# Kernel tuning notes

Measured on AMD Instinct MI355X. Metric: run time of the kernel, lower is better.

The kernel has to match this reference:

```python
import jax, jax.numpy as jnp
import numpy as np

B, S, D_MODEL, D_MEM, N_HEADS, NU = 8, 2048, 1024, 1024, 16, 3
D_HEAD = D_MODEL // N_HEADS            # 64
D_KEY = 2 * NU * (D_MEM // N_HEADS)    # 384


def _to_heads(x, n_heads):
    b, s, d = x.shape
    return x.reshape(b, s, n_heads, d // n_heads).transpose(0, 2, 1, 3)


def _dpfp(x, nu):
    # Deterministic Positive Feature Projection: (..., d) -> (..., 2*nu*d)
    x = jnp.concatenate([jax.nn.relu(x), jax.nn.relu(-x)], axis=-1)
    rolled = jnp.concatenate([jnp.roll(x, j, axis=-1) for j in range(1, nu + 1)], axis=-1)
    rep = jnp.concatenate([x] * nu, axis=-1)
    return rep * rolled


def setup_inputs() -> dict:
    key = jax.random.key(0)
    k0, k1, k2, k3, k4 = jax.random.split(key, 5)
    mem_tokens = jax.random.normal(k0, (B, S, D_MODEL), dtype=jnp.float32)
    # nn.Linear(in, out) weight shape is [out, in]
    W_mk = jax.random.normal(k1, (D_MEM, D_MODEL), dtype=jnp.float32) * 0.02
    W_mv = jax.random.normal(k2, (D_MODEL, D_MODEL), dtype=jnp.float32) * 0.02
    W_mb = jax.random.normal(k3, (D_MODEL, D_MODEL), dtype=jnp.float32) * 0.02
    W_mem = jax.random.normal(k4, (B, N_HEADS, D_KEY, D_HEAD), dtype=jnp.float32) * 0.01
    z = jnp.ones((B, N_HEADS, D_KEY), dtype=jnp.float32)
    return {"mem_tokens": mem_tokens, "W_mk": W_mk, "W_mv": W_mv, "W_mb": W_mb,
            "W_mem": W_mem, "z": z}


def reference(mem_tokens, W_mk, W_mv, W_mb, W_mem, z):
    # key projection + DPFP feature map
    k = _to_heads(mem_tokens @ W_mk.T, N_HEADS)          # [b,h,s,d_mem/h]
    mk = _dpfp(k, NU)                                     # [b,h,s,d_key]
    norm = jnp.linalg.norm(mk, axis=-1, keepdims=True)
    mk = mk / jnp.maximum(norm, 1e-12)                    # F.normalize(p=2)

    new_mv = _to_heads(mem_tokens @ W_mv.T, N_HEADS)      # [b,h,s,d_head]

    # retrieve previous values (first_seg=False, use_denom=True path)
    num = jnp.einsum('bhsk,bhkd->bhsd', mk, W_mem)
    denom = jnp.einsum('bhk,bhsk->bhs', z, mk)[..., None] + 1e-5
    prev_mv = num / denom

    mv = new_mv - prev_mv
    mb = _to_heads(jax.nn.sigmoid(mem_tokens @ W_mb.T), N_HEADS)

    # gating=True einsum: 'ihjk,ihjt,ihjt->ihkt'
    associations = jnp.einsum('bhsk,bhsd,bhsd->bhkd', mk, mv, mb)
    return W_mem + associations
```

## Files before the change

kernel.cpp:

```cpp
#include <hip/hip_runtime.h>
#include <hip/hip_bf16.h>

#define B_ 8
#define S_ 2048
#define DM 1024
#define H_ 16
#define DH 64
#define DK 384

#define AS3 __attribute__((address_space(3)))
#define AS1 __attribute__((address_space(1)))
typedef unsigned int u32;

typedef __attribute__((ext_vector_type(8))) short bf16x8;
typedef __attribute__((ext_vector_type(4))) short bf16x4;
typedef __attribute__((ext_vector_type(4))) float f32x4;

static __device__ __forceinline__ ushort f2b(float f) {
  __hip_bfloat16 h = __float2bfloat16(f);
  return *reinterpret_cast<ushort*>(&h);
}
static __device__ __forceinline__ float b2f(ushort u) {
  __hip_bfloat16 h;
  *reinterpret_cast<ushort*>(&h) = u;
  return __bfloat162float(h);
}

__global__ __launch_bounds__(256) void k_cvt(
    const float* __restrict__ X, const float* __restrict__ Wk,
    const float* __restrict__ Wv, const float* __restrict__ Wb,
    ushort* __restrict__ Xb, ushort* __restrict__ Wball) {
  const int total = 2097152 + 3 * 131072;
  int c = blockIdx.x * 256 + threadIdx.x;
  const int stride = gridDim.x * 256;
  for (; c < total; c += stride) {
    const float* s;
    ushort* d;
    size_t off;
    if (c < 2097152) { s = X; d = Xb; off = (size_t)c; }
    else {
      int cc = c - 2097152;
      int wsel = cc >> 17;
      off = (size_t)(cc & 131071);
      s = wsel == 0 ? Wk : (wsel == 1 ? Wv : Wb);
      d = Wball + (size_t)wsel * (DM * DM);
    }
    float4 a = *(const float4*)(s + off * 8);
    float4 b = *(const float4*)(s + off * 8 + 4);
    ushort u[8] = { f2b(a.x), f2b(a.y), f2b(a.z), f2b(a.w),
                    f2b(b.x), f2b(b.y), f2b(b.z), f2b(b.w) };
    *(uint4*)(d + off * 8) = *(uint4*)u;
  }
}

__global__ __launch_bounds__(256) void k_proj(
    const ushort* __restrict__ Xb, const ushort* __restrict__ Wball,
    ushort* __restrict__ kvb) {
  __shared__ ushort SH[4 * 8192];
  const int t = threadIdx.x, lane = t & 63, w = t >> 6;
  const int wm = w >> 1, wn = w & 1;
  const int l15 = lane & 15, lq = lane >> 4;
  const int bid = blockIdx.x + (blockIdx.y << 7) + (blockIdx.z << 10);
  const int c = bid & 7, r = bid >> 3;
  const int zb = r >> 7;
  const int rem = r & 127;
  const int mgrp = rem >> 3;
  const int nb = rem & 7;
  const int m0 = (c * 16 + mgrp) * 128;
  const int n0 = nb * 128;
  const int wsel = zb;
  const ushort* Wmat = Wball + (size_t)wsel * (DM * DM);
  ushort* out = kvb + (size_t)wsel * ((size_t)B_ * H_ * S_ * DH);

  const int rowst = (lane >> 3);
  const int colsw = ((lane & 7) ^ rowst) << 3;

  const ushort* pX[4];
  const ushort* pW[4];
  #pragma unroll
  for (int j = 0; j < 4; j++) {
    int row = (w * 4 + j) * 8 + rowst;
    pX[j] = Xb + (size_t)(m0 + row) * DM + colsw;
    pW[j] = Wmat + (size_t)(n0 + row) * DM + colsw;
  }
  ushort* dA = SH + w * 2048;
  ushort* dB = SH + 16384 + w * 2048;

  auto STAGE = [&](int buf, int kidx) {
    #pragma unroll
    for (int j = 0; j < 4; j++) {
      __builtin_amdgcn_global_load_lds(
          (const AS1 u32*)(pX[j] + kidx * 64),
          (AS3 u32*)(dA + buf * 8192 + j * 512), 16, 0, 0);
      __builtin_amdgcn_global_load_lds(
          (const AS1 u32*)(pW[j] + kidx * 64),
          (AS3 u32*)(dB + buf * 8192 + j * 512), 16, 0, 0);
    }
  };

  const int aoffb = (wm * 64 + l15) * 64;
  const int boffb = (wn * 64 + l15) * 64;
  const int csw0 = (lq ^ (lane & 7)) << 3;
  const int csw1 = ((lq + 4) ^ (lane & 7)) << 3;

  f32x4 acc[4][4] = {};
  STAGE(0, 0);
  __syncthreads();
  #pragma unroll
  for (int kt = 0; kt < 16; kt++) {
    const int cur = kt & 1;
    if (kt < 15) STAGE(cur ^ 1, kt + 1);
    const int ab = cur * 8192;
    #pragma unroll
    for (int kk2 = 0; kk2 < 2; kk2++) {
      const int csw = kk2 ? csw1 : csw0;
      bf16x8 af[4], bfr[4];
      #pragma unroll
      for (int mi = 0; mi < 4; mi++)
        af[mi] = *(const bf16x8*)&SH[ab + aoffb + mi * 1024 + csw];
      #pragma unroll
      for (int ni = 0; ni < 4; ni++)
        bfr[ni] = *(const bf16x8*)&SH[16384 + ab + boffb + ni * 1024 + csw];
      #pragma unroll
      for (int mi = 0; mi < 4; mi++)
        #pragma unroll
        for (int ni = 0; ni < 4; ni++)
          acc[mi][ni] = __builtin_amdgcn_mfma_f32_16x16x32_bf16(af[mi], bfr[ni], acc[mi][ni], 0, 0, 0);
    }
    __syncthreads();
  }

  ushort (*Cb)[136] = (ushort (*)[136])SH;
  #pragma unroll
  for (int mi = 0; mi < 4; mi++)
    #pragma unroll
    for (int ni = 0; ni < 4; ni++)
      #pragma unroll
      for (int rr = 0; rr < 4; rr++) {
        float val = acc[mi][ni][rr];
        if (wsel == 2) val = 1.0f / (1.0f + __expf(-val));
        Cb[wm * 64 + mi * 16 + lq * 4 + rr][wn * 64 + ni * 16 + l15] = f2b(val);
      }
  __syncthreads();
  #pragma unroll
  for (int q = 0; q < 8; q++) {
    int idx = q * 256 + t;
    int lm = idx >> 4;
    int c16 = idx & 15;
    int m = m0 + lm;
    int b = m >> 11, s = m & 2047;
    int o0 = n0 + c16 * 8;
    int h = o0 >> 6, d = o0 & 63;
    *(uint4*)(out + (((size_t)(b * H_ + h)) * S_ + s) * DH + d) =
        *(uint4*)&Cb[lm][c16 * 8];
  }
}

__global__ __launch_bounds__(512) void k_fused6(
    const ushort* __restrict__ Kb, const ushort* __restrict__ Vb,
    const ushort* __restrict__ Bgb, const float* __restrict__ Wmem,
    const float* __restrict__ z, ushort* __restrict__ part) {
  __shared__ u32 mkLd[32][192];
  __shared__ ushort mkT[384][36];
  __shared__ ushort gLT[64][36];
  __shared__ ushort zL[384];
  const int t = threadIdx.x, l = t & 63, w = t >> 6;
  const int l15 = l & 15, lq = l >> 4;
  const int bh = blockIdx.y, seg = blockIdx.x;
  const size_t rowbase = (size_t)bh * S_;
  const int mi = w >> 2, ni = w & 3;
  const int dcol = ni * 16 + l15;

  for (int cc = t; cc < DK; cc += 512) {
    int u = cc >> 7, p = (cc & 127) >> 1, par = cc & 1;
    zL[cc] = f2b(z[(size_t)bh * DK + u * 128 + par * 64 + p]);
  }

  const float* Wm = Wmem + (size_t)bh * (DK * DH);
  bf16x8 bw[12];
  #pragma unroll
  for (int k0i = 0; k0i < 12; k0i++) {
    bf16x8 tmp;
    #pragma unroll
    for (int j = 0; j < 8; j++) {
      int cc = k0i * 32 + lq * 8 + j;
      int u = cc >> 7, p = (cc & 127) >> 1, par = cc & 1;
      tmp[j] = (short)f2b(Wm[(size_t)(u * 128 + par * 64 + p) * DH + dcol]);
    }
    bw[k0i] = tmp;
  }

  f32x4 acc[3][4] = {};
  ushort kreg[4], vreg[4], breg[4];

  auto LOADCH = [&](int ch) {
    const int s0 = seg * 512 + ch * 32;
    #pragma unroll
    for (int r = 0; r < 4; r++)
      kreg[r] = Kb[(rowbase + s0 + w * 4 + r) * DH + l];
    #pragma unroll
    for (int rr = 0; rr < 4; rr++) {
      size_t ga = (rowbase + s0 + mi * 16 + lq * 4 + rr) * DH + dcol;
      vreg[rr] = Vb[ga];
      breg[rr] = Bgb[ga];
    }
  };

  LOADCH(0);
  __syncthreads();

  for (int ch = 0; ch < 16; ch++) {
    float xpv[4], xnv[4];
    u32 pks[4];
    #pragma unroll
    for (int r = 0; r < 4; r++) {
      float kv = b2f(kreg[r]);
      xpv[r] = fmaxf(kv, 0.f);
      xnv[r] = fmaxf(-kv, 0.f);
      pks[r] = (u32)f2b(xpv[r]) | ((u32)f2b(xnv[r]) << 16);
    }
    ushort4 mp[6];
    #pragma unroll
    for (int u = 0; u < 3; u++) {
      int ie = (l - u - 1) & 127;
      int sl = ie & 63;
      bool sw = ie >= 64;
      #pragma unroll
      for (int r = 0; r < 4; r++) {
        u32 pp = (u32)__shfl((int)pks[r], sl);
        float ps = b2f((ushort)(pp & 0xffff));
        float ns = b2f((ushort)(pp >> 16));
        float xbe = sw ? ns : ps;
        float xbo = sw ? ps : ns;
        ushort bve = f2b(xpv[r] * xbe);
        ushort bvo = f2b(xnv[r] * xbo);
        int row = w * 4 + r;
        mkLd[row][(u * 64 + l) ^ ((row & 7) << 2)] = (u32)bve | ((u32)bvo << 16);
        ((ushort*)&mp[2 * u])[r] = bve;
        ((ushort*)&mp[2 * u + 1])[r] = bvo;
      }
    }
    #pragma unroll
    for (int tt = 0; tt < 6; tt++)
      *(ushort4*)&mkT[l + 64 * tt][w * 4] = mp[tt];
    __syncthreads();

    const u32* mkrow = &mkLd[mi * 16 + l15][0];
    const int xr = (l15 & 7) << 2;
    f32x4 an0 = {}, an1 = {}, gacc = {}, zacc = {};
    #pragma unroll
    for (int k0i = 0; k0i < 12; k0i += 2) {
      bf16x8 afA = *(const bf16x8*)(mkrow + ((k0i * 16 + lq * 4) ^ xr));
      bf16x8 afB = *(const bf16x8*)(mkrow + (((k0i + 1) * 16 + lq * 4) ^ xr));
      bf16x8 zfA = *(const bf16x8*)&zL[k0i * 32 + lq * 8];
      bf16x8 zfB = *(const bf16x8*)&zL[(k0i + 1) * 32 + lq * 8];
      an0 = __builtin_amdgcn_mfma_f32_16x16x32_bf16(afA, bw[k0i], an0, 0, 0, 0);
      an1 = __builtin_amdgcn_mfma_f32_16x16x32_bf16(afB, bw[k0i + 1], an1, 0, 0, 0);
      gacc = __builtin_amdgcn_mfma_f32_16x16x32_bf16(afA, afA, gacc, 0, 0, 0);
      gacc = __builtin_amdgcn_mfma_f32_16x16x32_bf16(afB, afB, gacc, 0, 0, 0);
      zacc = __builtin_amdgcn_mfma_f32_16x16x32_bf16(afA, zfA, zacc, 0, 0, 0);
      zacc = __builtin_amdgcn_mfma_f32_16x16x32_bf16(afB, zfB, zacc, 0, 0, 0);
    }
    f32x4 an = an0 + an1;
    float ssqv[4];
    #pragma unroll
    for (int rr = 0; rr < 4; rr++)
      ssqv[rr] = __shfl(gacc[rr], (lq << 4) + lq * 4 + rr);
    {
      ushort4 gp;
      #pragma unroll
      for (int rr = 0; rr < 4; rr++) {
        float inv = 1.0f / fmaxf(sqrtf(ssqv[rr]), 1e-12f);
        float rden = 1.0f / (inv * zacc[rr] + 1e-5f);
        float prev = an[rr] * inv * rden;
        float g = (b2f(vreg[rr]) - prev) * b2f(breg[rr]);
        ((ushort*)&gp)[rr] = f2b(g * inv);
      }
      *(ushort4*)&gLT[dcol][mi * 16 + lq * 4] = gp;
    }
    __syncthreads();

    if (ch < 15) LOADCH(ch + 1);

    {
      bf16x8 bfr[4];
      #pragma unroll
      for (int n2 = 0; n2 < 4; n2++) {
        bf16x4 blo = *(const bf16x4*)&gLT[n2 * 16 + l15][lq * 8];
        bf16x4 bhi = *(const bf16x4*)&gLT[n2 * 16 + l15][lq * 8 + 4];
        bfr[n2] = __builtin_shufflevector(blo, bhi, 0, 1, 2, 3, 4, 5, 6, 7);
      }
      #pragma unroll
      for (int m2 = 0; m2 < 3; m2++) {
        bf16x4 alo = *(const bf16x4*)&mkT[w * 48 + m2 * 16 + l15][lq * 8];
        bf16x4 ahi = *(const bf16x4*)&mkT[w * 48 + m2 * 16 + l15][lq * 8 + 4];
        bf16x8 af = __builtin_shufflevector(alo, ahi, 0, 1, 2, 3, 4, 5, 6, 7);
        #pragma unroll
        for (int n2 = 0; n2 < 4; n2++)
          acc[m2][n2] = __builtin_amdgcn_mfma_f32_16x16x32_bf16(af, bfr[n2], acc[m2][n2], 0, 0, 0);
      }
    }
    __syncthreads();
  }

  ushort* pb = part + ((size_t)bh * 4 + seg) * (DK * DH);
  #pragma unroll
  for (int m2 = 0; m2 < 3; m2++)
    #pragma unroll
    for (int n2 = 0; n2 < 4; n2++)
      #pragma unroll
      for (int rc = 0; rc < 4; rc++)
        pb[(size_t)(w * 48 + m2 * 16 + lq * 4 + rc) * DH + n2 * 16 + l15] =
            f2b(acc[m2][n2][rc]);
}

__global__ __launch_bounds__(256) void k_reduce(
    const float* __restrict__ Wmem, const ushort* __restrict__ part,
    float* __restrict__ out) {
  size_t i4 = (size_t)blockIdx.x * 256 + threadIdx.x;
  int bh = (int)(i4 / 6144);
  size_t r4 = i4 - (size_t)bh * 6144;
  float4 acc = *(const float4*)(Wmem + i4 * 4);
  #pragma unroll
  for (int k = 0; k < 4; k++) {
    const ushort* pp = part + ((size_t)bh * 4 + k) * (DK * DH) + r4 * 4;
    ushort4 pv = *(const ushort4*)pp;
    acc.x += b2f(pv.x);
    acc.y += b2f(pv.y);
    acc.z += b2f(pv.z);
    acc.w += b2f(pv.w);
  }
  *(float4*)(out + i4 * 4) = acc;
}

extern "C" void kernel_launch(void* const* d_in, const int* in_sizes, int n_in,
                              void* d_out, int out_size, void* d_ws, size_t ws_size,
                              hipStream_t stream) {
  const float* X  = (const float*)d_in[0];
  const float* Wk = (const float*)d_in[1];
  const float* Wv = (const float*)d_in[2];
  const float* Wb = (const float*)d_in[3];
  const float* Wm = (const float*)d_in[4];
  const float* z  = (const float*)d_in[5];
  float* out = (float*)d_out;
  char* ws = (char*)d_ws;

  ushort* Xb    = (ushort*)(ws);
  ushort* Wball = (ushort*)(ws + 33554432ull);
  ushort* kvb   = (ushort*)(ws + 39845888ull);
  ushort* part  = (ushort*)(ws);
  ushort* Kb  = kvb;
  ushort* Vb  = kvb + (size_t)B_ * H_ * S_ * DH;
  ushort* Bgb = kvb + 2ull * (size_t)B_ * H_ * S_ * DH;

  k_cvt   <<<dim3(2048), 256, 0, stream>>>(X, Wk, Wv, Wb, Xb, Wball);
  k_proj  <<<dim3(128, 8, 3), 256, 0, stream>>>(Xb, Wball, kvb);
  k_fused6<<<dim3(4, B_ * H_), 512, 0, stream>>>(Kb, Vb, Bgb, Wm, z, part);
  k_reduce<<<dim3(3072), 256, 0, stream>>>(Wm, part, out);
}
```

Measured before the change: 245.8 us.

## Enlarge projection GEMM tile to 256x128 with 8 waves and triple-buffered LDS

The projection GEMM moves from 128x128 tiles with 4 waves to 256x128 tiles with 8 waves, so each block reuses its weight tile across twice as many rows. It also goes from double to triple buffering, using explicit vmcnt waits and a single barrier per k-step, so loads run two stages ahead. This cuts redundant global reads and barrier stalls, at the cost of more LDS per block (144KB), lower occupancy and fewer blocks in the grid.

```diff
diff --git a/kernel.cpp b/kernel.cpp
--- a/kernel.cpp
+++ b/kernel.cpp
@@ -53,82 +53,84 @@
   }
 }
 
-__global__ __launch_bounds__(256) void k_proj(
+__global__ __launch_bounds__(512) void k_proj(
     const ushort* __restrict__ Xb, const ushort* __restrict__ Wball,
     ushort* __restrict__ kvb) {
-  __shared__ ushort SH[4 * 8192];
+  __shared__ ushort SH[3 * 24576];
   const int t = threadIdx.x, lane = t & 63, w = t >> 6;
   const int wm = w >> 1, wn = w & 1;
   const int l15 = lane & 15, lq = lane >> 4;
-  const int bid = blockIdx.x + (blockIdx.y << 7) + (blockIdx.z << 10);
+  const int bid = blockIdx.x + (blockIdx.y << 6) + (blockIdx.z << 9);
   const int c = bid & 7, r = bid >> 3;
-  const int zb = r >> 7;
-  const int rem = r & 127;
+  const int zb = r >> 6;
+  const int rem = r & 63;
   const int mgrp = rem >> 3;
   const int nb = rem & 7;
-  const int m0 = (c * 16 + mgrp) * 128;
+  const int m0 = (c * 8 + mgrp) * 256;
   const int n0 = nb * 128;
   const int wsel = zb;
   const ushort* Wmat = Wball + (size_t)wsel * (DM * DM);
   ushort* out = kvb + (size_t)wsel * ((size_t)B_ * H_ * S_ * DH);
 
-  const int rowst = (lane >> 3);
-  const int colsw = ((lane & 7) ^ rowst) << 3;
-
-  const ushort* pX[4];
-  const ushort* pW[4];
-  #pragma unroll
-  for (int j = 0; j < 4; j++) {
-    int row = (w * 4 + j) * 8 + rowst;
-    pX[j] = Xb + (size_t)(m0 + row) * DM + colsw;
-    pW[j] = Wmat + (size_t)(n0 + row) * DM + colsw;
-  }
-  ushort* dA = SH + w * 2048;
-  ushort* dB = SH + 16384 + w * 2048;
+  const int srow = t >> 3;
+  const int scol8 = ((t & 7) ^ (srow & 7)) * 8;
+
+  const ushort* pA[4];
+  const ushort* pB[2];
+  #pragma unroll
+  for (int j = 0; j < 4; j++)
+    pA[j] = Xb + (size_t)(m0 + j * 64 + srow) * DM + scol8;
+  #pragma unroll
+  for (int j = 0; j < 2; j++)
+    pB[j] = Wmat + (size_t)(n0 + j * 64 + srow) * DM + scol8;
 
   auto STAGE = [&](int buf, int kidx) {
-    #pragma unroll
-    for (int j = 0; j < 4; j++) {
+    ushort* base = SH + buf * 24576;
+    #pragma unroll
+    for (int j = 0; j < 4; j++)
       __builtin_amdgcn_global_load_lds(
-          (const AS1 u32*)(pX[j] + kidx * 64),
-          (AS3 u32*)(dA + buf * 8192 + j * 512), 16, 0, 0);
+          (const AS1 u32*)(pA[j] + kidx * 64),
+          (AS3 u32*)(base + j * 4096 + t * 8), 16, 0, 0);
+    #pragma unroll
+    for (int j = 0; j < 2; j++)
       __builtin_amdgcn_global_load_lds(
-          (const AS1 u32*)(pW[j] + kidx * 64),
-          (AS3 u32*)(dB + buf * 8192 + j * 512), 16, 0, 0);
-    }
+          (const AS1 u32*)(pB[j] + kidx * 64),
+          (AS3 u32*)(base + 16384 + j * 4096 + t * 8), 16, 0, 0);
   };
 
   const int aoffb = (wm * 64 + l15) * 64;
-  const int boffb = (wn * 64 + l15) * 64;
+  const int boffb = 16384 + (wn * 64 + l15) * 64;
   const int csw0 = (lq ^ (lane & 7)) << 3;
   const int csw1 = ((lq + 4) ^ (lane & 7)) << 3;
 
   f32x4 acc[4][4] = {};
   STAGE(0, 0);
-  __syncthreads();
+  STAGE(1, 1);
   #pragma unroll
   for (int kt = 0; kt < 16; kt++) {
-    const int cur = kt & 1;
-    if (kt < 15) STAGE(cur ^ 1, kt + 1);
-    const int ab = cur * 8192;
+    if (kt < 15) asm volatile("s_waitcnt vmcnt(6)" ::: "memory");
+    else         asm volatile("s_waitcnt vmcnt(0)" ::: "memory");
+    __builtin_amdgcn_s_barrier();
+    if (kt < 14) STAGE((kt + 2) % 3, kt + 2);
+    const ushort* Ab = SH + (kt % 3) * 24576;
     #pragma unroll
     for (int kk2 = 0; kk2 < 2; kk2++) {
       const int csw = kk2 ? csw1 : csw0;
       bf16x8 af[4], bfr[4];
       #pragma unroll
       for (int mi = 0; mi < 4; mi++)
-        af[mi] = *(const bf16x8*)&SH[ab + aoffb + mi * 1024 + csw];
+        af[mi] = *(const bf16x8*)&Ab[aoffb + mi * 1024 + csw];
       #pragma unroll
       for (int ni = 0; ni < 4; ni++)
-        bfr[ni] = *(const bf16x8*)&SH[16384 + ab + boffb + ni * 1024 + csw];
+        bfr[ni] = *(const bf16x8*)&Ab[boffb + ni * 1024 + csw];
       #pragma unroll
       for (int mi = 0; mi < 4; mi++)
         #pragma unroll
         for (int ni = 0; ni < 4; ni++)
           acc[mi][ni] = __builtin_amdgcn_mfma_f32_16x16x32_bf16(af[mi], bfr[ni], acc[mi][ni], 0, 0, 0);
     }
-    __syncthreads();
-  }
+  }
+  __syncthreads();
 
   ushort (*Cb)[136] = (ushort (*)[136])SH;
   #pragma unroll
@@ -144,7 +146,7 @@
   __syncthreads();
   #pragma unroll
   for (int q = 0; q < 8; q++) {
-    int idx = q * 256 + t;
+    int idx = q * 512 + t;
     int lm = idx >> 4;
     int c16 = idx & 15;
     int m = m0 + lm;
@@ -354,7 +356,7 @@
   ushort* Bgb = kvb + 2ull * (size_t)B_ * H_ * S_ * DH;
 
   k_cvt   <<<dim3(2048), 256, 0, stream>>>(X, Wk, Wv, Wb, Xb, Wball);
-  k_proj  <<<dim3(128, 8, 3), 256, 0, stream>>>(Xb, Wball, kvb);
+  k_proj  <<<dim3(64, 8, 3), 512, 0, stream>>>(Xb, Wball, kvb);
   k_fused6<<<dim3(4, B_ * H_), 512, 0, stream>>>(Kb, Vb, Bgb, Wm, z, part);
   k_reduce<<<dim3(3072), 256, 0, stream>>>(Wm, part, out);
 }
```

Result: no change. 241.1 us (-1.9%).
